# Kernel optimization log

Measured on AMD Instinct MI355X. Metric: run time of the kernel, lower is better.

Reference implementation:

```python
import jax, jax.numpy as jnp
import numpy as np

N_NODES = 100000


def gcn_conv(x, edge_index, W, b):
    # PyG GCNConv: add self-loops, symmetric normalization D^-1/2 (A+I) D^-1/2,
    # linear transform then scatter-add aggregation at target nodes, plus bias.
    n = x.shape[0]
    loops = jnp.arange(n, dtype=edge_index.dtype)
    src = jnp.concatenate([edge_index[0], loops])
    dst = jnp.concatenate([edge_index[1], loops])
    deg = jax.ops.segment_sum(jnp.ones_like(dst, dtype=x.dtype), dst, num_segments=n)
    dinv = jnp.where(deg > 0, jax.lax.rsqrt(deg), 0.0)
    norm = dinv[src] * dinv[dst]  # [E+N]
    h = x @ W                      # transform first (small out dim)
    msg = h[src] * norm[:, None]   # per-edge gather + scale
    out = jax.ops.segment_sum(msg, dst, num_segments=n)
    return out + b


def setup_inputs() -> dict:
    key = jax.random.key(0)
    k1, k2, k3, k4 = jax.random.split(key, 4)
    N, E = N_NODES, 3200000
    x = jax.random.normal(k1, (N, 132), dtype=jnp.float32)
    edge_index = jax.random.randint(k2, (2, E), 0, N, dtype=jnp.int64)
    W1 = jax.random.normal(k3, (132, 16), dtype=jnp.float32) * 0.1
    b1 = jnp.zeros((16,), dtype=jnp.float32)
    W2 = jax.random.normal(k4, (16, 10), dtype=jnp.float32) * 0.25
    b2 = jnp.zeros((10,), dtype=jnp.float32)
    return {"x": x, "edge_index": edge_index, "W1": W1, "b1": b1, "W2": W2, "b2": b2}


def reference(x, edge_index, W1, b1, W2, b2):
    h = gcn_conv(x, edge_index, W1, b1)
    h = jax.nn.relu(h)
    # F.dropout(training=self.training) is identity in eval mode
    h = gcn_conv(h, edge_index, W2, b2)
    return jax.nn.log_softmax(h, axis=1)
```

## Files before the change

kernel.cpp:

```cpp
#include <hip/hip_runtime.h>
#include <math.h>


#define F_IN 132
#define F1   16
#define F2   10
#define BSH  7
#define BSPAN 128
#define NB   782
#define CAP  4608
#define SPB  6272
#define SPLIT_BLOCKS 512

__device__ __forceinline__ unsigned short f2bf(float f) {
    unsigned u = __float_as_uint(f);
    u += 0x7FFFu + ((u >> 16) & 1u);
    return (unsigned short)(u >> 16);
}
__device__ __forceinline__ float bflo(unsigned u) { return __uint_as_float(u << 16); }
__device__ __forceinline__ float bfhi(unsigned u) { return __uint_as_float(u & 0xFFFF0000u); }

__global__ __launch_bounds__(1024) void k_split(const int* __restrict__ src,
                                                const int* __restrict__ dst,
                                                int* __restrict__ gcur,
                                                unsigned* __restrict__ entries, int E) {
    __shared__ unsigned le[SPB];
    __shared__ int h0[1024];
    __shared__ int h1[1024];
    __shared__ int off[NB];
    __shared__ int wsum[16];
    const int t = threadIdx.x;
    const int lane = t & 63, wv = t >> 6;
    const int lo = blockIdx.x * SPB;
    const int hi = min(E, lo + SPB);
    int n = hi - lo; if (n < 0) n = 0;
    const int n4 = n >> 2;
    h0[t] = 0;
    __syncthreads();
    const int4* d4 = (const int4*)(dst + lo);
    const int4* s4 = (const int4*)(src + lo);
    for (int i = t; i < n4; i += 1024) {
        int4 d = d4[i];
        atomicAdd(&h0[d.x >> BSH], 1);
        atomicAdd(&h0[d.y >> BSH], 1);
        atomicAdd(&h0[d.z >> BSH], 1);
        atomicAdd(&h0[d.w >> BSH], 1);
    }
    __syncthreads();
    int c = h0[t];
    int v = c;
    #pragma unroll
    for (int o = 1; o < 64; o <<= 1) {
        int u = __shfl_up(v, o, 64);
        if (lane >= o) v += u;
    }
    if (lane == 63) wsum[wv] = v;
    __syncthreads();
    if (wv == 0) {
        int s = (lane < 16) ? wsum[lane] : 0;
        #pragma unroll
        for (int o = 1; o < 16; o <<= 1) {
            int u = __shfl_up(s, o, 64);
            if (lane >= o) s += u;
        }
        if (lane < 16) wsum[lane] = s;
    }
    __syncthreads();
    v += wv ? wsum[wv - 1] : 0;
    h1[t] = v;
    int excl = v - c;
    if (t < NB) {
        int g = t * CAP + (c ? atomicAdd(&gcur[t], c) : 0);
        off[t] = g - excl;
    }
    h0[t] = excl;
    __syncthreads();
    for (int i = t; i < n4; i += 1024) {
        int4 d = d4[i];
        int4 s = s4[i];
        int p;
        p = atomicAdd(&h0[d.x >> BSH], 1); le[p] = ((unsigned)(d.x & 127) << 17) | (unsigned)s.x;
        p = atomicAdd(&h0[d.y >> BSH], 1); le[p] = ((unsigned)(d.y & 127) << 17) | (unsigned)s.y;
        p = atomicAdd(&h0[d.z >> BSH], 1); le[p] = ((unsigned)(d.z & 127) << 17) | (unsigned)s.z;
        p = atomicAdd(&h0[d.w >> BSH], 1); le[p] = ((unsigned)(d.w & 127) << 17) | (unsigned)s.w;
    }
    __syncthreads();
    for (int bk = t; bk < NB; bk += 1024) {
        int s0 = bk ? h1[bk - 1] : 0;
        int e0 = h1[bk];
        unsigned* gp = entries + off[bk] + s0;
        for (int i = s0; i < e0; ++i) *gp++ = le[i];
    }
}

__global__ void k_sortB(const int* __restrict__ gcur, unsigned* __restrict__ entries,
                        int* __restrict__ rps, int* __restrict__ rpe,
                        float* __restrict__ dinv, int N) {
    __shared__ unsigned le[CAP];
    __shared__ int hist4[4][BSPAN];
    __shared__ int cur[BSPAN];
    __shared__ int ws2[2];
    const int b = blockIdx.x;
    const int t = threadIdx.x;
    const int lane = t & 63, wv = t >> 6;
    const int cbase = b * CAP;
    const int cnt = gcur[b];
    for (int i = t; i < 4 * BSPAN; i += 256) ((int*)hist4)[i] = 0;
    __syncthreads();
    for (int i = t; i < cnt; i += 256) {
        unsigned p = entries[cbase + i];
        le[i] = p;
        atomicAdd(&hist4[wv][p >> 17], 1);
    }
    __syncthreads();
    int h = 0, v = 0;
    if (t < BSPAN) {
        h = hist4[0][t] + hist4[1][t] + hist4[2][t] + hist4[3][t];
        v = h;
        #pragma unroll
        for (int o = 1; o < 64; o <<= 1) {
            int u = __shfl_up(v, o, 64);
            if (lane >= o) v += u;
        }
        if (lane == 63) ws2[wv] = v;
    }
    __syncthreads();
    if (t < BSPAN) {
        if (wv == 1) v += ws2[0];
        const int node = b * BSPAN + t;
        const int begl = v - h;
        cur[t] = cbase + begl;
        if (node < N) {
            rps[node] = cbase + begl;
            rpe[node] = cbase + begl + h;
            dinv[node] = rsqrtf((float)h + 1.0f);
        }
    }
    __syncthreads();
    for (int i = t; i < cnt; i += 256) {
        unsigned p = le[i];
        int pos = atomicAdd(&cur[p >> 17], 1);
        entries[pos] = p & 0x1FFFFu;
    }
}

__global__ void k_xw1(const float* __restrict__ x, const float* __restrict__ W1,
                      const float* __restrict__ dinv, unsigned short* __restrict__ g1u, int N) {
    __shared__ float xs[16 * F_IN];
    __shared__ float wsm[F_IN * F1];
    const int t = threadIdx.x;
    const int base = blockIdx.x * 16;
    for (int idx = t; idx < 528; idx += 256)
        ((float4*)wsm)[idx] = ((const float4*)W1)[idx];
    int nrows = N - base; if (nrows > 16) nrows = 16;
    const float4* xp4 = (const float4*)(x + (size_t)base * F_IN);
    const int span4 = nrows * 33;
    for (int idx = t; idx < span4; idx += 256) ((float4*)xs)[idx] = xp4[idx];
    __syncthreads();
    const int r = t >> 4;
    const int c = t & 15;
    if (r < nrows) {
        float acc = 0.f;
        #pragma unroll 4
        for (int k = 0; k < F_IN; ++k) acc += xs[r * F_IN + k] * wsm[k * F1 + c];
        g1u[(size_t)(base + r) * 16 + c] = f2bf(acc * dinv[base + r]);
    }
}

#define ACCU8(qv, B) \
    acc[(B)+0] += bflo((qv).x); acc[(B)+1] += bfhi((qv).x); \
    acc[(B)+2] += bflo((qv).y); acc[(B)+3] += bfhi((qv).y); \
    acc[(B)+4] += bflo((qv).z); acc[(B)+5] += bfhi((qv).z); \
    acc[(B)+6] += bflo((qv).w); acc[(B)+7] += bfhi((qv).w);

__global__ void k_agg1(const int* __restrict__ rps, const int* __restrict__ rpe,
                       const unsigned* __restrict__ ssrc, const unsigned short* __restrict__ g1u,
                       const float* __restrict__ dinv, const float* __restrict__ b1,
                       const float* __restrict__ W2, unsigned short* __restrict__ g2u, int N) {
    __shared__ float w2s[F1 * F2];
    __shared__ float b1s[F1];
    if (threadIdx.x < F1 * F2) w2s[threadIdx.x] = W2[threadIdx.x];
    if (threadIdx.x < F1) b1s[threadIdx.x] = b1[threadIdx.x];
    __syncthreads();
    const int gid = blockIdx.x * blockDim.x + threadIdx.x;
    const int d = gid >> 3;
    const int q = gid & 7;
    if (d >= N) return;
    const int beg = rps[d], end = rpe[d];
    float acc[F1];
    #pragma unroll
    for (int j = 0; j < F1; ++j) acc[j] = 0.f;
    int e = beg + q;
    for (; e + 8 < end; e += 16) {
        int s0 = (int)ssrc[e];
        int s1 = (int)ssrc[e + 8];
        const uint4* r0 = (const uint4*)(g1u + (size_t)s0 * 16);
        const uint4* r1 = (const uint4*)(g1u + (size_t)s1 * 16);
        uint4 a0 = r0[0], a1 = r0[1];
        uint4 c0 = r1[0], c1 = r1[1];
        ACCU8(a0, 0) ACCU8(a1, 8)
        ACCU8(c0, 0) ACCU8(c1, 8)
    }
    if (e < end) {
        int s = (int)ssrc[e];
        const uint4* r = (const uint4*)(g1u + (size_t)s * 16);
        uint4 a0 = r[0], a1 = r[1];
        ACCU8(a0, 0) ACCU8(a1, 8)
    }
    if (q == 0) {
        const uint4* r = (const uint4*)(g1u + (size_t)d * 16);
        uint4 a0 = r[0], a1 = r[1];
        ACCU8(a0, 0) ACCU8(a1, 8)
    }
    #pragma unroll
    for (int j = 0; j < F1; ++j) acc[j] += __shfl_xor(acc[j], 1);
    #pragma unroll
    for (int j = 0; j < F1; ++j) acc[j] += __shfl_xor(acc[j], 2);
    #pragma unroll
    for (int j = 0; j < F1; ++j) acc[j] += __shfl_xor(acc[j], 4);
    if (q == 0) {
        const float dv = dinv[d];
        float tt[F1];
        #pragma unroll
        for (int j = 0; j < F1; ++j) {
            float v = dv * acc[j] + b1s[j];
            tt[j] = v > 0.f ? v : 0.f;
        }
        float o[F2];
        #pragma unroll
        for (int c = 0; c < F2; ++c) {
            float a = 0.f;
            #pragma unroll
            for (int j = 0; j < F1; ++j) a += tt[j] * w2s[j * F2 + c];
            o[c] = dv * a;
        }
        unsigned w0 = ((unsigned)f2bf(o[1]) << 16) | f2bf(o[0]);
        unsigned w1 = ((unsigned)f2bf(o[3]) << 16) | f2bf(o[2]);
        unsigned w2 = ((unsigned)f2bf(o[5]) << 16) | f2bf(o[4]);
        unsigned w3 = ((unsigned)f2bf(o[7]) << 16) | f2bf(o[6]);
        unsigned w4 = ((unsigned)f2bf(o[9]) << 16) | f2bf(o[8]);
        uint4* op = (uint4*)(g2u + (size_t)d * 16);
        op[0] = make_uint4(w0, w1, w2, w3);
        op[1] = make_uint4(w4, 0u, 0u, 0u);
    }
}

__global__ void k_agg2(const int* __restrict__ rps, const int* __restrict__ rpe,
                       const unsigned* __restrict__ ssrc, const unsigned short* __restrict__ g2u,
                       const float* __restrict__ dinv, const float* __restrict__ b2,
                       float* __restrict__ out, int N) {
    __shared__ float b2s[F2];
    if (threadIdx.x < F2) b2s[threadIdx.x] = b2[threadIdx.x];
    __syncthreads();
    const int gid = blockIdx.x * blockDim.x + threadIdx.x;
    const int d = gid >> 3;
    const int q = gid & 7;
    if (d >= N) return;
    const int beg = rps[d], end = rpe[d];
    float acc[F2];
    #pragma unroll
    for (int c = 0; c < F2; ++c) acc[c] = 0.f;
    int e = beg + q;
    for (; e + 8 < end; e += 16) {
        int s0 = (int)ssrc[e];
        int s1 = (int)ssrc[e + 8];
        const unsigned short* p0 = g2u + (size_t)s0 * 16;
        const unsigned short* p1 = g2u + (size_t)s1 * 16;
        uint4 a0 = *(const uint4*)(p0);
        unsigned a4 = *(const unsigned*)(p0 + 8);
        uint4 c0 = *(const uint4*)(p1);
        unsigned c4 = *(const unsigned*)(p1 + 8);
        ACCU8(a0, 0)
        acc[8] += bflo(a4); acc[9] += bfhi(a4);
        ACCU8(c0, 0)
        acc[8] += bflo(c4); acc[9] += bfhi(c4);
    }
    if (e < end) {
        int s = (int)ssrc[e];
        const unsigned short* p = g2u + (size_t)s * 16;
        uint4 a0 = *(const uint4*)(p);
        unsigned a4 = *(const unsigned*)(p + 8);
        ACCU8(a0, 0)
        acc[8] += bflo(a4); acc[9] += bfhi(a4);
    }
    if (q == 0) {
        const unsigned short* p = g2u + (size_t)d * 16;
        uint4 a0 = *(const uint4*)(p);
        unsigned a4 = *(const unsigned*)(p + 8);
        ACCU8(a0, 0)
        acc[8] += bflo(a4); acc[9] += bfhi(a4);
    }
    #pragma unroll
    for (int c = 0; c < F2; ++c) acc[c] += __shfl_xor(acc[c], 1);
    #pragma unroll
    for (int c = 0; c < F2; ++c) acc[c] += __shfl_xor(acc[c], 2);
    #pragma unroll
    for (int c = 0; c < F2; ++c) acc[c] += __shfl_xor(acc[c], 4);
    if (q == 0) {
        const float dv = dinv[d];
        float v[F2];
        float m = -INFINITY;
        #pragma unroll
        for (int c = 0; c < F2; ++c) {
            v[c] = dv * acc[c] + b2s[c];
            m = fmaxf(m, v[c]);
        }
        float ssum = 0.f;
        #pragma unroll
        for (int c = 0; c < F2; ++c) ssum += expf(v[c] - m);
        float ls = logf(ssum);
        float* op = out + (size_t)d * F2;
        *(float4*)(op)     = make_float4(v[0]-m-ls, v[1]-m-ls, v[2]-m-ls, v[3]-m-ls);
        *(float4*)(op + 4) = make_float4(v[4]-m-ls, v[5]-m-ls, v[6]-m-ls, v[7]-m-ls);
        *(float2*)(op + 8) = make_float2(v[8]-m-ls, v[9]-m-ls);
    }
}

extern "C" void kernel_launch(void* const* d_in, const int* in_sizes, int n_in,
                              void* d_out, int out_size, void* d_ws, size_t ws_size,
                              hipStream_t stream) {
    const float* x  = (const float*)d_in[0];
    const int*   ei = (const int*)  d_in[1];
    const float* W1 = (const float*)d_in[2];
    const float* b1 = (const float*)d_in[3];
    const float* W2 = (const float*)d_in[4];
    const float* b2 = (const float*)d_in[5];
    float* out = (float*)d_out;

    const int N = in_sizes[0] / F_IN;
    const int E = in_sizes[1] / 2;
    const int* src = ei;
    const int* dst = ei + E;

    char* w = (char*)d_ws;
    int*            gcur    = (int*)w;            w += ((size_t)NB * 4 + 255) & ~255ull;
    int*            rps     = (int*)w;            w += ((size_t)N * 4 + 255) & ~255ull;
    int*            rpe     = (int*)w;            w += ((size_t)N * 4 + 255) & ~255ull;
    float*          dinv    = (float*)w;          w += ((size_t)N * 4 + 255) & ~255ull;
    unsigned short* g1u     = (unsigned short*)w; w += ((size_t)N * 16 * 2 + 255) & ~255ull;
    unsigned short* g2u     = (unsigned short*)w; w += ((size_t)N * 16 * 2 + 255) & ~255ull;
    unsigned*       entries = (unsigned*)w;

    (void)hipMemsetAsync(gcur, 0, (size_t)NB * 4, stream);
    k_split<<<SPLIT_BLOCKS, 1024, 0, stream>>>(src, dst, gcur, entries, E);
    k_sortB<<<NB, 256, 0, stream>>>(gcur, entries, rps, rpe, dinv, N);
    k_xw1  <<<(N + 15) / 16, 256, 0, stream>>>(x, W1, dinv, g1u, N);
    k_agg1 <<<(8 * N + 255) / 256, 256, 0, stream>>>(rps, rpe, entries, g1u, dinv, b1, W2, g2u, N);
    k_agg2 <<<(8 * N + 255) / 256, 256, 0, stream>>>(rps, rpe, entries, g2u, dinv, b2, out, N);
}
```

Measured before the change: 141.7 us.

## Degree-sort nodes within buckets for aggregation balance; enlarge split chunks

k_sortB now builds a per-bucket permutation that orders the 128 nodes of each bucket by in-degree (capped at 127) using a shared-memory counting sort. k_agg1 and k_agg2 read a node id from this permutation, so the 8-lane groups in each wavefront handle nodes of similar degree, which is meant to cut divergence and tail imbalance. The split kernel now uses 256 blocks of 12500 edges instead of 512 blocks of 6272. That halves the global atomics on the bucket cursors but raises LDS use per block. The wave-shuffle prefix scan in k_split is replaced by a simpler Hillis-Steele shared-memory scan, which needs more barriers.

```diff
diff --git a/kernel.cpp b/kernel.cpp
--- a/kernel.cpp
+++ b/kernel.cpp
@@ -9,8 +9,8 @@
 #define BSPAN 128
 #define NB   782
 #define CAP  4608
-#define SPB  6272
-#define SPLIT_BLOCKS 512
+#define SPB  12500
+#define SPLIT_BLOCKS 256
 
 __device__ __forceinline__ unsigned short f2bf(float f) {
     unsigned u = __float_as_uint(f);
@@ -28,13 +28,10 @@
     __shared__ int h0[1024];
     __shared__ int h1[1024];
     __shared__ int off[NB];
-    __shared__ int wsum[16];
     const int t = threadIdx.x;
-    const int lane = t & 63, wv = t >> 6;
     const int lo = blockIdx.x * SPB;
     const int hi = min(E, lo + SPB);
-    int n = hi - lo; if (n < 0) n = 0;
-    const int n4 = n >> 2;
+    const int n4 = (hi - lo) >> 2;
     h0[t] = 0;
     __syncthreads();
     const int4* d4 = (const int4*)(dst + lo);
@@ -48,27 +45,15 @@
     }
     __syncthreads();
     int c = h0[t];
-    int v = c;
-    #pragma unroll
-    for (int o = 1; o < 64; o <<= 1) {
-        int u = __shfl_up(v, o, 64);
-        if (lane >= o) v += u;
-    }
-    if (lane == 63) wsum[wv] = v;
-    __syncthreads();
-    if (wv == 0) {
-        int s = (lane < 16) ? wsum[lane] : 0;
-        #pragma unroll
-        for (int o = 1; o < 16; o <<= 1) {
-            int u = __shfl_up(s, o, 64);
-            if (lane >= o) s += u;
-        }
-        if (lane < 16) wsum[lane] = s;
-    }
-    __syncthreads();
-    v += wv ? wsum[wv - 1] : 0;
-    h1[t] = v;
-    int excl = v - c;
+    h1[t] = c;
+    __syncthreads();
+    for (int o = 1; o < 1024; o <<= 1) {
+        int v = (t >= o) ? h1[t - o] : 0;
+        __syncthreads();
+        h1[t] += v;
+        __syncthreads();
+    }
+    int excl = h1[t] - c;
     if (t < NB) {
         int g = t * CAP + (c ? atomicAdd(&gcur[t], c) : 0);
         off[t] = g - excl;
@@ -95,17 +80,20 @@
 
 __global__ void k_sortB(const int* __restrict__ gcur, unsigned* __restrict__ entries,
                         int* __restrict__ rps, int* __restrict__ rpe,
-                        float* __restrict__ dinv, int N) {
+                        float* __restrict__ dinv, int* __restrict__ perm, int N) {
     __shared__ unsigned le[CAP];
     __shared__ int hist4[4][BSPAN];
     __shared__ int cur[BSPAN];
-    __shared__ int ws2[2];
+    __shared__ int dbin[BSPAN];
+    __shared__ int dcur[BSPAN];
+    __shared__ int ws2[2], ws3[2];
     const int b = blockIdx.x;
     const int t = threadIdx.x;
     const int lane = t & 63, wv = t >> 6;
     const int cbase = b * CAP;
     const int cnt = gcur[b];
     for (int i = t; i < 4 * BSPAN; i += 256) ((int*)hist4)[i] = 0;
+    if (t < BSPAN) dbin[t] = 0;
     __syncthreads();
     for (int i = t; i < cnt; i += 256) {
         unsigned p = entries[cbase + i];
@@ -123,8 +111,10 @@
             if (lane >= o) v += u;
         }
         if (lane == 63) ws2[wv] = v;
-    }
-    __syncthreads();
+        if (b * BSPAN + t < N) atomicAdd(&dbin[min(h, BSPAN - 1)], 1);
+    }
+    __syncthreads();
+    int dc = 0, dvv = 0;
     if (t < BSPAN) {
         if (wv == 1) v += ws2[0];
         const int node = b * BSPAN + t;
@@ -134,6 +124,27 @@
             rps[node] = cbase + begl;
             rpe[node] = cbase + begl + h;
             dinv[node] = rsqrtf((float)h + 1.0f);
+        }
+        dc = dbin[t];
+        dvv = dc;
+        #pragma unroll
+        for (int o = 1; o < 64; o <<= 1) {
+            int u = __shfl_up(dvv, o, 64);
+            if (lane >= o) dvv += u;
+        }
+        if (lane == 63) ws3[wv] = dvv;
+    }
+    __syncthreads();
+    if (t < BSPAN) {
+        if (wv == 1) dvv += ws3[0];
+        dcur[t] = dvv - dc;
+    }
+    __syncthreads();
+    if (t < BSPAN) {
+        const int node = b * BSPAN + t;
+        if (node < N) {
+            int r = atomicAdd(&dcur[min(h, BSPAN - 1)], 1);
+            perm[b * BSPAN + r] = node;
         }
     }
     __syncthreads();
@@ -176,16 +187,18 @@
 __global__ void k_agg1(const int* __restrict__ rps, const int* __restrict__ rpe,
                        const unsigned* __restrict__ ssrc, const unsigned short* __restrict__ g1u,
                        const float* __restrict__ dinv, const float* __restrict__ b1,
-                       const float* __restrict__ W2, unsigned short* __restrict__ g2u, int N) {
+                       const float* __restrict__ W2, unsigned short* __restrict__ g2u,
+                       const int* __restrict__ perm, int N) {
     __shared__ float w2s[F1 * F2];
     __shared__ float b1s[F1];
     if (threadIdx.x < F1 * F2) w2s[threadIdx.x] = W2[threadIdx.x];
     if (threadIdx.x < F1) b1s[threadIdx.x] = b1[threadIdx.x];
     __syncthreads();
     const int gid = blockIdx.x * blockDim.x + threadIdx.x;
-    const int d = gid >> 3;
+    const int nid = gid >> 3;
     const int q = gid & 7;
-    if (d >= N) return;
+    if (nid >= N) return;
+    const int d = perm[nid];
     const int beg = rps[d], end = rpe[d];
     float acc[F1];
     #pragma unroll
@@ -248,14 +261,15 @@
 __global__ void k_agg2(const int* __restrict__ rps, const int* __restrict__ rpe,
                        const unsigned* __restrict__ ssrc, const unsigned short* __restrict__ g2u,
                        const float* __restrict__ dinv, const float* __restrict__ b2,
-                       float* __restrict__ out, int N) {
+                       float* __restrict__ out, const int* __restrict__ perm, int N) {
     __shared__ float b2s[F2];
     if (threadIdx.x < F2) b2s[threadIdx.x] = b2[threadIdx.x];
     __syncthreads();
     const int gid = blockIdx.x * blockDim.x + threadIdx.x;
-    const int d = gid >> 3;
+    const int nid = gid >> 3;
     const int q = gid & 7;
-    if (d >= N) return;
+    if (nid >= N) return;
+    const int d = perm[nid];
     const int beg = rps[d], end = rpe[d];
     float acc[F2];
     #pragma unroll
@@ -337,14 +351,15 @@
     int*            rps     = (int*)w;            w += ((size_t)N * 4 + 255) & ~255ull;
     int*            rpe     = (int*)w;            w += ((size_t)N * 4 + 255) & ~255ull;
     float*          dinv    = (float*)w;          w += ((size_t)N * 4 + 255) & ~255ull;
+    int*            perm    = (int*)w;            w += ((size_t)N * 4 + 255) & ~255ull;
     unsigned short* g1u     = (unsigned short*)w; w += ((size_t)N * 16 * 2 + 255) & ~255ull;
     unsigned short* g2u     = (unsigned short*)w; w += ((size_t)N * 16 * 2 + 255) & ~255ull;
     unsigned*       entries = (unsigned*)w;
 
     (void)hipMemsetAsync(gcur, 0, (size_t)NB * 4, stream);
     k_split<<<SPLIT_BLOCKS, 1024, 0, stream>>>(src, dst, gcur, entries, E);
-    k_sortB<<<NB, 256, 0, stream>>>(gcur, entries, rps, rpe, dinv, N);
+    k_sortB<<<NB, 256, 0, stream>>>(gcur, entries, rps, rpe, dinv, perm, N);
     k_xw1  <<<(N + 15) / 16, 256, 0, stream>>>(x, W1, dinv, g1u, N);
-    k_agg1 <<<(8 * N + 255) / 256, 256, 0, stream>>>(rps, rpe, entries, g1u, dinv, b1, W2, g2u, N);
-    k_agg2 <<<(8 * N + 255) / 256, 256, 0, stream>>>(rps, rpe, entries, g2u, dinv, b2, out, N);
-}
+    k_agg1 <<<(8 * N + 255) / 256, 256, 0, stream>>>(rps, rpe, entries, g1u, dinv, b1, W2, g2u, perm, N);
+    k_agg2 <<<(8 * N + 255) / 256, 256, 0, stream>>>(rps, rpe, entries, g2u, dinv, b2, out, perm, N);
+}
```

After: 148.1 us. +4.5%, slower.
